# Kernel tuning notes

Hardware: AMD Instinct MI355X
Metric: run time of the kernel (lower is better)

## Reference

```python
import jax, jax.numpy as jnp
import numpy as np
from jax import lax

N_BOXES = 6000
IOU_THR = 0.5
CONF_THR = 0.6


def setup_inputs() -> dict:
    key = jax.random.key(0)
    k1, k2, k3 = jax.random.split(key, 3)
    # valid xyxy boxes: top-left in [0,1000), width/height in [1,101)
    xy = jax.random.uniform(k1, (N_BOXES, 2), dtype=jnp.float32) * 1000.0
    wh = jax.random.uniform(k2, (N_BOXES, 2), dtype=jnp.float32) * 100.0 + 1.0
    boxes = jnp.concatenate([xy, xy + wh], axis=-1)  # [N,4] x1,y1,x2,y2
    scores = jax.random.uniform(k3, (N_BOXES,), dtype=jnp.float32)
    return {"boxes": boxes, "scores": scores}


def _pairwise_iou(b):
    # b: [N,4] xyxy. Returns [N,N] IoU, coordinates handled separately to
    # avoid materializing [N,N,2] intermediates.
    x1, y1, x2, y2 = b[:, 0], b[:, 1], b[:, 2], b[:, 3]
    area = (x2 - x1) * (y2 - y1)  # [N]
    iw = jnp.clip(jnp.minimum(x2[:, None], x2[None, :]) - jnp.maximum(x1[:, None], x1[None, :]), 0.0)
    ih = jnp.clip(jnp.minimum(y2[:, None], y2[None, :]) - jnp.maximum(y1[:, None], y1[None, :]), 0.0)
    inter = iw * ih  # [N,N]
    return inter / (area[:, None] + area[None, :] - inter)


def reference(boxes, scores):
    """torchvision-style NMS (suppress IoU > 0.5) then confidence filter (>= 0.6).
    Returns masked scores [N]: score where the box survives both stages, else 0.
    (Fixed-shape mask form of the original index outputs, for jit compatibility.)
    """
    n = scores.shape[0]
    order = jnp.argsort(-scores)  # descending by confidence
    iou = _pairwise_iou(boxes[order])  # [N,N] in sorted order
    idx = jnp.arange(n)

    def body(suppressed, i):
        keep_i = jnp.logical_not(suppressed[i])
        # a kept box suppresses all lower-scoring boxes with IoU > threshold
        supp_new = keep_i & (iou[i] > IOU_THR) & (idx > i)
        return suppressed | supp_new, keep_i

    _, keep_sorted = lax.scan(body, jnp.zeros((n,), dtype=bool), idx)
    keep = jnp.zeros((n,), dtype=bool).at[order].set(keep_sorted)
    final = keep & (scores >= CONF_THR)
    return jnp.where(final, scores, 0.0)
```

## Files before the change

### kernel.cpp

```cpp
#include <hip/hip_runtime.h>
#include <stdint.h>

#define N_BOXES 6000
#define NT 94
#define NROWS (NT * 64)
#define CAP 64
#define IOU_THR 0.5f
#define CONF_THR 0.6f

typedef unsigned long long u64;
typedef unsigned int u32;
typedef unsigned short u16;

#define BAR() asm volatile("s_waitcnt lgkmcnt(0)\n\ts_barrier" ::: "memory")

__device__ __forceinline__ u64 rdlane64(u64 v, int l) {
    unsigned lo = (unsigned)__builtin_amdgcn_readlane((int)(unsigned)v, l);
    unsigned hi = (unsigned)__builtin_amdgcn_readlane((int)(unsigned)(v >> 32), l);
    return ((u64)hi << 32) | lo;
}

__global__ void __launch_bounds__(1024) k_sort(const float* __restrict__ scores,
                                               const float4* __restrict__ boxes,
                                               int* __restrict__ sidx,
                                               float4* __restrict__ sboxes,
                                               u32* __restrict__ lists_w,
                                               int* __restrict__ cnt) {
    __shared__ u64 kt[N_BOXES];
    __shared__ int part[1024];
    const int tid = threadIdx.x;
    const int gtid = blockIdx.x * 1024 + tid;
    for (int j = gtid; j < NROWS * CAP / 2; j += NT * 1024) lists_w[j] = 0xFFFFFFFFu;
    for (int j = gtid; j < NROWS; j += NT * 1024) cnt[j] = 0;

    for (int j = tid; j < N_BOXES; j += 1024) {
        unsigned inv = ~__float_as_uint(scores[j]);
        kt[j] = ((u64)inv << 32) | (unsigned)j;
    }
    __syncthreads();
    const int il = tid & 63;
    const int i = blockIdx.x * 64 + il;
    const int j0 = (tid >> 6) * 375;
    u64 mykey = (i < N_BOXES) ? kt[i] : 0ull;
    int cntr = 0;
#pragma unroll 5
    for (int jj = 0; jj < 375; ++jj)
        cntr += (kt[j0 + jj] < mykey) ? 1 : 0;
    part[tid] = cntr;
    __syncthreads();
    if (tid < 64 && i < N_BOXES) {
        int r = 0;
#pragma unroll
        for (int s = 0; s < 16; ++s) r += part[il + 64 * s];
        sidx[r] = i;
        sboxes[r] = boxes[i];
    }
}

__global__ void k_mask(const float4* __restrict__ sboxes,
                       u16* __restrict__ lists, int* __restrict__ cnt,
                       u64* __restrict__ diagw) {
    int ct = blockIdx.x, rt = blockIdx.y;
    if (ct < rt) return;
    int lane = threadIdx.x;
    __shared__ float4 rb[64];
    int row0 = rt * 64;
    int rows = min(64, N_BOXES - row0);
    if (lane < rows) rb[lane] = sboxes[row0 + lane];
    __syncthreads();
    int j = ct * 64 + lane;
    bool jvalid = (j < N_BOXES);
    float4 cb = make_float4(0.f, 0.f, 1.f, 1.f);
    if (jvalid) cb = sboxes[j];
    float carea = (cb.z - cb.x) * (cb.w - cb.y);
    bool isdiag = (ct == rt);
    for (int i = 0; i < rows; ++i) {
        float4 rbx = rb[i];
        float rarea = (rbx.z - rbx.x) * (rbx.w - rbx.y);
        float iw = fmaxf(fminf(rbx.z, cb.z) - fmaxf(rbx.x, cb.x), 0.f);
        float ih = fmaxf(fminf(rbx.w, cb.w) - fmaxf(rbx.y, cb.y), 0.f);
        float inter = iw * ih;
        float iou = inter / ((rarea + carea) - inter);
        int row = row0 + i;
        bool pred = jvalid && (j > row) && (iou > IOU_THR);
        if (isdiag) {
            u64 bal = __ballot(pred);
            if (lane == (i & 63)) diagw[row] = bal;
        } else if (pred) {
            int slot = atomicAdd(&cnt[row], 1);
            if (slot < CAP) lists[row * CAP + slot] = (u16)j;
        }
    }
}

__global__ void __launch_bounds__(1024) k_scan(const u16* __restrict__ lists,
                                               const u64* __restrict__ diagw,
                                               const int* __restrict__ sidx,
                                               const float* __restrict__ scores,
                                               float* __restrict__ out) {
    __shared__ u64 removed[NT];
    __shared__ u64 kwbuf[NT];
    const int tid   = threadIdx.x;
    const int lane  = tid & 63;
    const int row_l = tid >> 4;
    const int sg    = (tid & 15) * 4;
    if (tid < NT) removed[tid] = 0;

    u64 LA, LB, dA, dB;
    LA = *(const u64*)&lists[(0 * 64 + row_l) * CAP + sg];
    dA = diagw[lane];
    dB = 0;
    __syncthreads();

#define STEP(T, LUSE, LFILL, DUSE, DFILL)                                      \
    {                                                                          \
        const int tn = ((T) + 1 < NT) ? ((T) + 1) : 0;                         \
        LFILL = *(const u64*)&lists[(tn * 64 + row_l) * CAP + sg];             \
        DFILL = diagw[tn * 64 + lane];                           \
        const u64 nz = __ballot(DUSE != 0ull);        \
        const int row0 = (T) * 64;                                             \
        const int rows = (N_BOXES - row0 >= 64) ? 64 : (N_BOXES - row0);       \
        const u64 valid = (rows == 64) ? ~0ull : ((1ull << rows) - 1ull);      \
        u64 c = valid & ~removed[(T)];                                         \
        u64 kw = 0;                                                            \
        while (c) {                                                            \
            u64 blockers = c & nz;                                             \
            if (!blockers) { kw |= c; break; }             \
            int g = (int)__builtin_ctzll(blockers);                            \
            u64 below = c & ((1ull << g) - 1ull);         \
            kw |= below | (1ull << g);                                         \
            u64 df = rdlane64(DUSE, g);                     \
            c &= ~(df | below | (1ull << g));                                  \
        }                                                                      \
        if (tid == 0) kwbuf[(T)] = kw;                                         \
        if (((kw >> row_l) & 1ull) && LUSE != ~0ull) {                         \
            u16 e0 = (u16)(LUSE), e1 = (u16)(LUSE >> 16),                      \
                e2 = (u16)(LUSE >> 32), e3 = (u16)(LUSE >> 48);                \
            if (e0 != 0xFFFFu) atomicOr(&removed[e0 >> 6], 1ull << (e0 & 63)); \
            if (e1 != 0xFFFFu) atomicOr(&removed[e1 >> 6], 1ull << (e1 & 63)); \
            if (e2 != 0xFFFFu) atomicOr(&removed[e2 >> 6], 1ull << (e2 & 63)); \
            if (e3 != 0xFFFFu) atomicOr(&removed[e3 >> 6], 1ull << (e3 & 63)); \
        }                                                                      \
        BAR();                                                                 \
    }

    for (int t = 0; t < NT; t += 2) {
        STEP(t,     LA, LB, dA, dB)
        STEP(t + 1, LB, LA, dB, dA)
    }
#undef STEP

    for (int p = tid; p < N_BOXES; p += 1024) {
        int orig = sidx[p];
        float s = scores[orig];
        bool k = (kwbuf[p >> 6] >> (p & 63)) & 1ull;
        out[orig] = (k && (s >= CONF_THR)) ? s : 0.0f;
    }
}

extern "C" void kernel_launch(void* const* d_in, const int* in_sizes, int n_in,
                              void* d_out, int out_size, void* d_ws, size_t ws_size,
                              hipStream_t stream) {
    const float* boxes  = (const float*)d_in[0];
    const float* scores = (const float*)d_in[1];
    float* out = (float*)d_out;

    char* ws = (char*)d_ws;
    u16*    lists  = (u16*)(ws);
    int*    cnt    = (int*)(ws + 770048);
    u64*    diagw  = (u64*)(ws + 794112);
    int*    sidx   = (int*)(ws + 842240);
    float4* sboxes = (float4*)(ws + 866240);

    k_sort<<<dim3(NT), dim3(1024), 0, stream>>>(scores, (const float4*)boxes, sidx,
                                                sboxes, (u32*)lists, cnt);
    k_mask<<<dim3(NT, NT), dim3(64), 0, stream>>>((const float4*)sboxes, lists, cnt, diagw);
    k_scan<<<dim3(1), dim3(1024), 0, stream>>>(lists, diagw, sidx, scores, out);
}
```

Baseline: 142.4 us.

## Shrink scan block, cut list capacity, and deepen prefetch pipeline to three tiles

The single-block sequential scan drops from 1024 to 256 threads, and per-row suppression lists shrink from 64 to 16 entries. Each thread now handles four list entries of a row instead of all sixteen threads sharing it, which means fewer waves per barrier. Tile loads of lists and diagonal words are prefetched three tiles ahead, issued after the current tile's work, so global latency can hide behind more steps. The tile count is padded to 96 so the loop unrolls by three. The risk is that any row with more than 16 off-diagonal suppressions silently loses entries.

Result: faster. 132.7 us (-6.8%).

```diff
diff --git a/kernel.cpp b/kernel.cpp
--- a/kernel.cpp
+++ b/kernel.cpp
@@ -3,8 +3,9 @@
 
 #define N_BOXES 6000
 #define NT 94
-#define NROWS (NT * 64)
-#define CAP 64
+#define NTP 96
+#define NROWS (NTP * 64)
+#define CAP 16
 #define IOU_THR 0.5f
 #define CONF_THR 0.6f
 
@@ -93,34 +94,35 @@
     }
 }
 
-__global__ void __launch_bounds__(1024) k_scan(const u16* __restrict__ lists,
-                                               const u64* __restrict__ diagw,
-                                               const int* __restrict__ sidx,
-                                               const float* __restrict__ scores,
-                                               float* __restrict__ out) {
-    __shared__ u64 removed[NT];
-    __shared__ u64 kwbuf[NT];
+__global__ void __launch_bounds__(256) k_scan(const u16* __restrict__ lists,
+                                              const u64* __restrict__ diagw,
+                                              const int* __restrict__ sidx,
+                                              const float* __restrict__ scores,
+                                              float* __restrict__ out) {
+    __shared__ u64 removed[NTP];
+    __shared__ u64 kwbuf[NTP];
     const int tid   = threadIdx.x;
     const int lane  = tid & 63;
-    const int row_l = tid >> 4;
-    const int sg    = (tid & 15) * 4;
-    if (tid < NT) removed[tid] = 0;
+    const int row_l = tid >> 2;
+    const int sg    = (tid & 3) * 4;
+    if (tid < NTP) removed[tid] = 0;
 
-    u64 LA, LB, dA, dB;
-    LA = *(const u64*)&lists[(0 * 64 + row_l) * CAP + sg];
-    dA = diagw[lane];
-    dB = 0;
+    u64 L0, L1, L2, D0, D1, D2;
+    L0 = *(const u64*)&lists[(0 * 64 + row_l) * CAP + sg];
+    L1 = *(const u64*)&lists[(1 * 64 + row_l) * CAP + sg];
+    L2 = *(const u64*)&lists[(2 * 64 + row_l) * CAP + sg];
+    D0 = diagw[0 * 64 + lane];
+    D1 = diagw[1 * 64 + lane];
+    D2 = diagw[2 * 64 + lane];
     __syncthreads();
 
-#define STEP(T, LUSE, LFILL, DUSE, DFILL)                                      \
+#define STEP(T, LUSE, DUSE)                                                    \
     {                                                                          \
-        const int tn = ((T) + 1 < NT) ? ((T) + 1) : 0;                         \
-        LFILL = *(const u64*)&lists[(tn * 64 + row_l) * CAP + sg];             \
-        DFILL = diagw[tn * 64 + lane];                           \
         const u64 nz = __ballot(DUSE != 0ull);        \
         const int row0 = (T) * 64;                                             \
-        const int rows = (N_BOXES - row0 >= 64) ? 64 : (N_BOXES - row0);       \
-        const u64 valid = (rows == 64) ? ~0ull : ((1ull << rows) - 1ull);      \
+        const int rem = N_BOXES - row0;                                        \
+        const u64 valid = (rem >= 64) ? ~0ull                                  \
+                        : ((rem <= 0) ? 0ull : ((1ull << rem) - 1ull));        \
         u64 c = valid & ~removed[(T)];                                         \
         u64 kw = 0;                                                            \
         while (c) {                                                            \
@@ -141,16 +143,20 @@
             if (e2 != 0xFFFFu) atomicOr(&removed[e2 >> 6], 1ull << (e2 & 63)); \
             if (e3 != 0xFFFFu) atomicOr(&removed[e3 >> 6], 1ull << (e3 & 63)); \
         }                                                                      \
+        const int tn = ((T) + 3 < NTP) ? ((T) + 3) : ((T) + 3 - NTP);          \
+        LUSE = *(const u64*)&lists[(tn * 64 + row_l) * CAP + sg];              \
+        DUSE = diagw[tn * 64 + lane];                                          \
         BAR();                                                                 \
     }
 
-    for (int t = 0; t < NT; t += 2) {
-        STEP(t,     LA, LB, dA, dB)
-        STEP(t + 1, LB, LA, dB, dA)
+    for (int t = 0; t < NTP; t += 3) {
+        STEP(t,     L0, D0)
+        STEP(t + 1, L1, D1)
+        STEP(t + 2, L2, D2)
     }
 #undef STEP
 
-    for (int p = tid; p < N_BOXES; p += 1024) {
+    for (int p = tid; p < N_BOXES; p += 256) {
         int orig = sidx[p];
         float s = scores[orig];
         bool k = (kwbuf[p >> 6] >> (p & 63)) & 1ull;
@@ -167,13 +173,13 @@
 
     char* ws = (char*)d_ws;
     u16*    lists  = (u16*)(ws);
-    int*    cnt    = (int*)(ws + 770048);
-    u64*    diagw  = (u64*)(ws + 794112);
-    int*    sidx   = (int*)(ws + 842240);
-    float4* sboxes = (float4*)(ws + 866240);
+    int*    cnt    = (int*)(ws + 196608);
+    u64*    diagw  = (u64*)(ws + 221184);
+    int*    sidx   = (int*)(ws + 270336);
+    float4* sboxes = (float4*)(ws + 294336);
 
     k_sort<<<dim3(NT), dim3(1024), 0, stream>>>(scores, (const float4*)boxes, sidx,
                                                 sboxes, (u32*)lists, cnt);
     k_mask<<<dim3(NT, NT), dim3(64), 0, stream>>>((const float4*)sboxes, lists, cnt, diagw);
-    k_scan<<<dim3(1), dim3(1024), 0, stream>>>(lists, diagw, sidx, scores, out);
+    k_scan<<<dim3(1), dim3(256), 0, stream>>>(lists, diagw, sidx, scores, out);
 }
```

## Replace per-row suppression lists with global edge list bucketed in LDS

Applied to the files above, without the earlier changes.

Off-diagonal suppression pairs now go into one compact global edge array through a single atomic counter, replacing per-row fixed-capacity lists. This removes the large list-clearing pass in the sort kernel. The scan kernel loads the edges into LDS and buckets them by tile with a count, prefix-scan and scatter, then runs the serial greedy scan on a single wavefront with no block barriers. The cost is heavy contention on one global atomic counter in the mask kernel, plus extra setup work in the single-block scan. Edges beyond the fixed capacity are silently dropped.

New measurement: 141.2 us. Within noise of the previous version (-0.9%).

```diff
diff --git a/kernel.cpp b/kernel.cpp
--- a/kernel.cpp
+++ b/kernel.cpp
@@ -3,16 +3,15 @@
 
 #define N_BOXES 6000
 #define NT 94
-#define NROWS (NT * 64)
-#define CAP 64
+#define NROWS 6016
+#define ECAP 24576
 #define IOU_THR 0.5f
 #define CONF_THR 0.6f
 
 typedef unsigned long long u64;
 typedef unsigned int u32;
 typedef unsigned short u16;
-
-#define BAR() asm volatile("s_waitcnt lgkmcnt(0)\n\ts_barrier" ::: "memory")
+typedef unsigned char u8;
 
 __device__ __forceinline__ u64 rdlane64(u64 v, int l) {
     unsigned lo = (unsigned)__builtin_amdgcn_readlane((int)(unsigned)v, l);
@@ -24,15 +23,11 @@
                                                const float4* __restrict__ boxes,
                                                int* __restrict__ sidx,
                                                float4* __restrict__ sboxes,
-                                               u32* __restrict__ lists_w,
-                                               int* __restrict__ cnt) {
+                                               int* __restrict__ ecnt) {
     __shared__ u64 kt[N_BOXES];
     __shared__ int part[1024];
     const int tid = threadIdx.x;
-    const int gtid = blockIdx.x * 1024 + tid;
-    for (int j = gtid; j < NROWS * CAP / 2; j += NT * 1024) lists_w[j] = 0xFFFFFFFFu;
-    for (int j = gtid; j < NROWS; j += NT * 1024) cnt[j] = 0;
-
+    if (blockIdx.x == 0 && tid == 0) *ecnt = 0;
     for (int j = tid; j < N_BOXES; j += 1024) {
         unsigned inv = ~__float_as_uint(scores[j]);
         kt[j] = ((u64)inv << 32) | (unsigned)j;
@@ -58,7 +53,7 @@
 }
 
 __global__ void k_mask(const float4* __restrict__ sboxes,
-                       u16* __restrict__ lists, int* __restrict__ cnt,
+                       u32* __restrict__ edges, int* __restrict__ ecnt,
                        u64* __restrict__ diagw) {
     int ct = blockIdx.x, rt = blockIdx.y;
     if (ct < rt) return;
@@ -87,68 +82,87 @@
             u64 bal = __ballot(pred);
             if (lane == (i & 63)) diagw[row] = bal;
         } else if (pred) {
-            int slot = atomicAdd(&cnt[row], 1);
-            if (slot < CAP) lists[row * CAP + slot] = (u16)j;
+            int e = atomicAdd(ecnt, 1);
+            if (e < ECAP) edges[e] = ((u32)row << 16) | (u32)j;
         }
     }
 }
 
-__global__ void __launch_bounds__(1024) k_scan(const u16* __restrict__ lists,
+__global__ void __launch_bounds__(1024) k_scan(const u32* __restrict__ edges,
+                                               const int* __restrict__ ecnt,
                                                const u64* __restrict__ diagw,
                                                const int* __restrict__ sidx,
                                                const float* __restrict__ scores,
                                                float* __restrict__ out) {
-    __shared__ u64 removed[NT];
-    __shared__ u64 kwbuf[NT];
-    const int tid   = threadIdx.x;
-    const int lane  = tid & 63;
-    const int row_l = tid >> 4;
-    const int sg    = (tid & 15) * 4;
-    if (tid < NT) removed[tid] = 0;
+    __shared__ u64 ldiag[NROWS];
+    __shared__ u16 ccol[ECAP];
+    __shared__ u8  crl[ECAP];
+    __shared__ u32 tilestart[96], cursor[96], scanbuf[96];
+    __shared__ u64 removed[96];
+    __shared__ u64 kwbuf[96];
+    const int tid = threadIdx.x;
 
-    u64 LA, LB, dA, dB;
-    LA = *(const u64*)&lists[(0 * 64 + row_l) * CAP + sg];
-    dA = diagw[lane];
-    dB = 0;
+    if (tid < 96) { cursor[tid] = 0; removed[tid] = 0; }
+    for (int k = tid; k < NROWS; k += 1024) ldiag[k] = diagw[k];
+    __syncthreads();
+    const int ne = min(*ecnt, ECAP);
+    for (int k = tid; k < ne; k += 1024)
+        atomicAdd(&cursor[(edges[k] >> 16) >> 6], 1u);
+    __syncthreads();
+    u32 myc = (tid < 96) ? cursor[tid] : 0;
+    if (tid < 96) scanbuf[tid] = myc;
+    __syncthreads();
+    for (int off = 1; off < 96; off <<= 1) {
+        u32 v = 0;
+        if (tid < 96 && tid >= off) v = scanbuf[tid - off];
+        __syncthreads();
+        if (tid < 96) scanbuf[tid] += v;
+        __syncthreads();
+    }
+    if (tid < 96) {
+        u32 st = scanbuf[tid] - myc;
+        tilestart[tid] = st;
+        cursor[tid] = st;
+    }
+    __syncthreads();
+    for (int k = tid; k < ne; k += 1024) {
+        u32 e = edges[k];
+        u32 row = e >> 16, col = e & 0xFFFFu, t = row >> 6;
+        u32 slot = atomicAdd(&cursor[t], 1u);
+        ccol[slot] = (u16)col;
+        crl[slot]  = (u8)(row & 63u);
+    }
     __syncthreads();
 
-#define STEP(T, LUSE, LFILL, DUSE, DFILL)                                      \
-    {                                                                          \
-        const int tn = ((T) + 1 < NT) ? ((T) + 1) : 0;                         \
-        LFILL = *(const u64*)&lists[(tn * 64 + row_l) * CAP + sg];             \
-        DFILL = diagw[tn * 64 + lane];                           \
-        const u64 nz = __ballot(DUSE != 0ull);        \
-        const int row0 = (T) * 64;                                             \
-        const int rows = (N_BOXES - row0 >= 64) ? 64 : (N_BOXES - row0);       \
-        const u64 valid = (rows == 64) ? ~0ull : ((1ull << rows) - 1ull);      \
-        u64 c = valid & ~removed[(T)];                                         \
-        u64 kw = 0;                                                            \
-        while (c) {                                                            \
-            u64 blockers = c & nz;                                             \
-            if (!blockers) { kw |= c; break; }             \
-            int g = (int)__builtin_ctzll(blockers);                            \
-            u64 below = c & ((1ull << g) - 1ull);         \
-            kw |= below | (1ull << g);                                         \
-            u64 df = rdlane64(DUSE, g);                     \
-            c &= ~(df | below | (1ull << g));                                  \
-        }                                                                      \
-        if (tid == 0) kwbuf[(T)] = kw;                                         \
-        if (((kw >> row_l) & 1ull) && LUSE != ~0ull) {                         \
-            u16 e0 = (u16)(LUSE), e1 = (u16)(LUSE >> 16),                      \
-                e2 = (u16)(LUSE >> 32), e3 = (u16)(LUSE >> 48);                \
-            if (e0 != 0xFFFFu) atomicOr(&removed[e0 >> 6], 1ull << (e0 & 63)); \
-            if (e1 != 0xFFFFu) atomicOr(&removed[e1 >> 6], 1ull << (e1 & 63)); \
-            if (e2 != 0xFFFFu) atomicOr(&removed[e2 >> 6], 1ull << (e2 & 63)); \
-            if (e3 != 0xFFFFu) atomicOr(&removed[e3 >> 6], 1ull << (e3 & 63)); \
-        }                                                                      \
-        BAR();                                                                 \
+    if (tid < 64) {
+        const int lane = tid;
+        for (int t = 0; t < NT; ++t) {
+            const u64 d = ldiag[t * 64 + lane];
+            const u64 nz = __ballot(d != 0ull);
+            const int rem = N_BOXES - t * 64;
+            const u64 valid = (rem >= 64) ? ~0ull : ((1ull << rem) - 1ull);
+            u64 c = valid & ~removed[t];
+            u64 kw = 0;
+            while (c) {
+                u64 blockers = c & nz;
+                if (!blockers) { kw |= c; break; }
+                int g = (int)__builtin_ctzll(blockers);
+                u64 below = c & ((1ull << g) - 1ull);
+                kw |= below | (1ull << g);
+                u64 df = rdlane64(d, g);
+                c &= ~(df | below | (1ull << g));
+            }
+            if (lane == 0) kwbuf[t] = kw;
+            const u32 beg = tilestart[t], end = cursor[t];
+            for (u32 b = beg + lane; b < end; b += 64) {
+                if ((kw >> crl[b]) & 1ull) {
+                    u32 col = ccol[b];
+                    atomicOr(&removed[col >> 6], 1ull << (col & 63));
+                }
+            }
+        }
     }
-
-    for (int t = 0; t < NT; t += 2) {
-        STEP(t,     LA, LB, dA, dB)
-        STEP(t + 1, LB, LA, dB, dA)
-    }
-#undef STEP
+    __syncthreads();
 
     for (int p = tid; p < N_BOXES; p += 1024) {
         int orig = sidx[p];
@@ -166,14 +180,16 @@
     float* out = (float*)d_out;
 
     char* ws = (char*)d_ws;
-    u16*    lists  = (u16*)(ws);
-    int*    cnt    = (int*)(ws + 770048);
-    u64*    diagw  = (u64*)(ws + 794112);
-    int*    sidx   = (int*)(ws + 842240);
-    float4* sboxes = (float4*)(ws + 866240);
+    u32* edges  = (u32*)(ws);
+    int* ecnt   = (int*)(ws + 98304);
+    u64* diagw  = (u64*)(ws + 98320);
+    int* sidx   = (int*)(ws + 146448);
+    float4* sboxes = (float4*)(ws + 170448);
 
-    k_sort<<<dim3(NT), dim3(1024), 0, stream>>>(scores, (const float4*)boxes, sidx,
-                                                sboxes, (u32*)lists, cnt);
-    k_mask<<<dim3(NT, NT), dim3(64), 0, stream>>>((const float4*)sboxes, lists, cnt, diagw);
-    k_scan<<<dim3(1), dim3(1024), 0, stream>>>(lists, diagw, sidx, scores, out);
+    k_sort<<<dim3(NT), dim3(1024), 0, stream>>>(scores, (const float4*)boxes,
+                                                sidx, sboxes, ecnt);
+    k_mask<<<dim3(NT, NT), dim3(64), 0, stream>>>((const float4*)sboxes,
+                                                  edges, ecnt, diagw);
+    k_scan<<<dim3(1), dim3(1024), 0, stream>>>(edges, ecnt, diagw,
+                                               sidx, scores, out);
 }
```
